# Kernel optimization log

Hardware: AMD Instinct MI355X
Metric: run time of the kernel (lower is better)

Reference implementation:

```python
import jax, jax.numpy as jnp
import numpy as np

N_NODES = 50000
N_EDGES = 800000
D_FEAT = 128      # node feature dim
D_IN = 2 * D_FEAT # MLP input (concat of x_i and x_j - x_i)
D_OUT = 256


def setup_inputs() -> dict:
    key = jax.random.key(0)
    ks = jax.random.split(key, 8)
    x = jax.random.normal(ks[0], (N_NODES, D_FEAT), dtype=jnp.float32)
    edge_index = jax.random.randint(ks[1], (2, N_EDGES), 0, N_NODES, dtype=jnp.int64)
    s1 = 1.0 / np.sqrt(D_IN)
    s2 = 1.0 / np.sqrt(D_OUT)
    W1 = jax.random.uniform(ks[2], (D_IN, D_OUT), jnp.float32, -s1, s1)
    b1 = jax.random.uniform(ks[3], (D_OUT,), jnp.float32, -s1, s1)
    W2 = jax.random.uniform(ks[4], (D_OUT, D_OUT), jnp.float32, -s2, s2)
    b2 = jax.random.uniform(ks[5], (D_OUT,), jnp.float32, -s2, s2)
    W3 = jax.random.uniform(ks[6], (D_OUT, D_OUT), jnp.float32, -s2, s2)
    b3 = jax.random.uniform(ks[7], (D_OUT,), jnp.float32, -s2, s2)
    return {"x": x, "edge_index": edge_index, "W1": W1, "b1": b1,
            "W2": W2, "b2": b2, "W3": W3, "b3": b3}


def reference(x, edge_index, W1, b1, W2, b2, W3, b3):
    # EdgeConv: for edge (j -> i): msg = MLP(concat([x_i, x_j - x_i])); max-aggregate at i
    src, dst = edge_index[0], edge_index[1]
    x_i = x[dst]                       # [E, D_FEAT] target features
    x_j = x[src]                       # [E, D_FEAT] source features
    e = jnp.concatenate([x_i, x_j - x_i], axis=-1)  # [E, 2*D_FEAT]
    h = jax.nn.relu(e @ W1 + b1)
    h = jax.nn.relu(h @ W2 + b2)
    h = h @ W3 + b3                    # [E, D_OUT]
    out = jax.ops.segment_max(h, dst, num_segments=N_NODES)  # [N, D_OUT]
    # nodes with no incoming edges -> 0 (PyG scatter-max fill)
    return jnp.where(jnp.isfinite(out), out, jnp.zeros((), out.dtype))
```

## Files before the change

### kernel.cpp

```cpp
#include <hip/hip_runtime.h>
#include <stdint.h>


#define N_NODES 50000
#define N_EDGES 800000
#define EPB 64
#define NBLK 12500

typedef __attribute__((ext_vector_type(4))) float f32x4;
typedef __attribute__((ext_vector_type(8))) _Float16 f16x8;
typedef __attribute__((ext_vector_type(4))) unsigned int u32x4;
typedef __attribute__((ext_vector_type(2))) unsigned int u32x2;

__device__ __forceinline__ unsigned int pkrtz(float a, float b){
  auto p = __builtin_amdgcn_cvt_pkrtz(a, b);
  return __builtin_bit_cast(unsigned int, p);
}
__device__ __forceinline__ unsigned int f16bits(float f){
  _Float16 h = (_Float16)f;
  return (unsigned int)__builtin_bit_cast(unsigned short, h);
}
__device__ __forceinline__ unsigned int pkadd_relu(unsigned int a, unsigned int b){
  unsigned int s, r;
  asm("v_pk_add_f16 %0, %1, %2" : "=v"(s) : "v"(a), "v"(b));
  asm("v_pk_max_f16 %0, %1, %2" : "=v"(r) : "v"(s), "v"(0u));
  return r;
}
__device__ __forceinline__ unsigned int fmap(float f){
  unsigned int u = __builtin_bit_cast(unsigned int, f);
  return (u & 0x80000000u) ? ~u : (u | 0x80000000u);
}
__device__ __forceinline__ bool is64(const unsigned int* e){
  return (e[1] | e[3] | e[5] | e[7] | e[9] | e[11] | e[13] | e[15]) == 0u;
}

extern "C" __global__ void k_histw(const void* __restrict__ eidx, unsigned int* __restrict__ cnt,
                                   const float* __restrict__ W1, const float* __restrict__ W2,
                                   const float* __restrict__ W3,
                                   unsigned short* __restrict__ w2s, unsigned short* __restrict__ w3s,
                                   unsigned short* __restrict__ wdf){
  const int b = blockIdx.x;
  if (b < 3125){
    int i = b * 256 + threadIdx.x;
    int d = is64((const unsigned int*)eidx)
          ? (int)((const long long*)eidx)[N_EDGES + i]
          : ((const int*)eidx)[N_EDGES + i];
    atomicAdd(&cnt[d], 1u);
    return;
  }
  int t = (b - 3125) * 256 + threadIdx.x;
  if (t < 16384){
    const float* W = (t & 8192) ? W3 : W2;
    unsigned short* o = (t & 8192) ? w3s : w2s;
    int r = t & 8191, lane = r & 63, blk = r >> 6;
    int m  = (blk >> 3) * 16 + (lane & 15);
    int k0 = (blk & 7) * 32 + (lane >> 4) * 8;
    u32x4 ov;
    #pragma unroll
    for (int j = 0; j < 4; j++){
      unsigned int lo = f16bits(W[(size_t)(k0 + 2*j    ) * 256 + m]);
      unsigned int hi = f16bits(W[(size_t)(k0 + 2*j + 1) * 256 + m]);
      ov[j] = lo | (hi << 16);
    }
    *(u32x4*)(o + (size_t)r * 8) = ov;
  } else {
    int r = t - 16384, lane = r & 63, blk = r >> 6;
    int m  = (blk >> 2) * 16 + (lane & 15);
    int k0 = (blk & 3) * 32 + (lane >> 4) * 8;
    u32x4 ov;
    #pragma unroll
    for (int j = 0; j < 4; j++){
      float vlo, vhi;
      int ka = k0 + 2*j, kb = k0 + 2*j + 1;
      if (m < 256){
        vlo = W1[(size_t)ka * 256 + m] - W1[(size_t)(ka + 128) * 256 + m];
        vhi = W1[(size_t)kb * 256 + m] - W1[(size_t)(kb + 128) * 256 + m];
      } else {
        vlo = W1[(size_t)(ka + 128) * 256 + (m - 256)];
        vhi = W1[(size_t)(kb + 128) * 256 + (m - 256)];
      }
      ov[j] = f16bits(vlo) | (f16bits(vhi) << 16);
    }
    *(u32x4*)(wdf + (size_t)r * 8) = ov;
  }
}

extern "C" __global__ void k_psum(const unsigned int* __restrict__ cnt, unsigned int* __restrict__ bsum){
  __shared__ unsigned int red[4];
  const int b = blockIdx.x, t = threadIdx.x, i = b * 256 + t;
  unsigned int v = (i < N_NODES) ? cnt[i] : 0u;
  #pragma unroll
  for (int d = 32; d; d >>= 1) v += __shfl_down(v, d, 64);
  if ((t & 63) == 0) red[t >> 6] = v;
  __syncthreads();
  if (t == 0) bsum[b] = red[0] + red[1] + red[2] + red[3];
}
extern "C" __global__ void __launch_bounds__(256) k_bscan(const unsigned int* __restrict__ bsum,
                                                          unsigned int* __restrict__ bbase){
  __shared__ unsigned int s[256];
  const int t = threadIdx.x;
  unsigned int v = (t < 196) ? bsum[t] : 0u;
  s[t] = v; __syncthreads();
  for (int d = 1; d < 256; d <<= 1){
    unsigned int u = (t >= d) ? s[t - d] : 0u;
    __syncthreads(); s[t] += u; __syncthreads();
  }
  if (t < 196) bbase[t] = s[t] - v;
}
extern "C" __global__ void k_apply(const unsigned int* __restrict__ cnt,
                                   const unsigned int* __restrict__ bbase,
                                   unsigned int* __restrict__ off){
  __shared__ unsigned int s[256];
  const int b = blockIdx.x, t = threadIdx.x, i = b * 256 + t;
  unsigned int v = (i < N_NODES) ? cnt[i] : 0u;
  s[t] = v; __syncthreads();
  for (int d = 1; d < 256; d <<= 1){
    unsigned int u = (t >= d) ? s[t - d] : 0u;
    __syncthreads(); s[t] += u; __syncthreads();
  }
  if (i < N_NODES) off[i] = bbase[b] + s[t] - v;
}

extern "C" __global__ void __launch_bounds__(256) k_bucketac(
    const void* __restrict__ eidx, unsigned int* __restrict__ cur,
    unsigned int* __restrict__ sPair,
    const float* __restrict__ x, const unsigned short* __restrict__ wdf,
    const float* __restrict__ b1, unsigned short* __restrict__ acb){
  __shared__ unsigned char smx[16384];
  const int b = blockIdx.x;
  if (b < 3125){
    int i = b * 256 + threadIdx.x;
    int s, d;
    if (is64((const unsigned int*)eidx)){
      const long long* p = (const long long*)eidx;
      s = (int)p[i]; d = (int)p[N_EDGES + i];
    } else {
      const int* p = (const int*)eidx;
      s = p[i]; d = p[N_EDGES + i];
    }
    unsigned int pos = atomicAdd(&cur[d], 1u);
    sPair[pos] = (unsigned int)s | ((unsigned int)d << 16);
    return;
  }
  const int tid = threadIdx.x, lane = tid & 63, w = tid >> 6;
  const int n0 = (b - 3125) * 64;
  {
    const int nl = tid >> 2, q = tid & 3;
    int node = n0 + nl; if (node > N_NODES - 1) node = N_NODES - 1;
    const f32x4* xp = (const f32x4*)(x + (size_t)node * 128 + q * 32);
    unsigned char* base = smx + (((nl >> 4) * 256 + q * 64 + (nl & 15)) << 4);
    #pragma unroll
    for (int s = 0; s < 4; s++){
      f32x4 v0 = xp[s * 2], v1 = xp[s * 2 + 1];
      u32x4 ov = { pkrtz(v0[0], v0[1]), pkrtz(v0[2], v0[3]),
                   pkrtz(v1[0], v1[1]), pkrtz(v1[2], v1[3]) };
      *(u32x4*)(base + s * 256) = ov;
    }
  }
  __syncthreads();
  const int lm = lane & 15, g = lane >> 4;
  f32x4 acc[8][4];
  #pragma unroll
  for (int mf = 0; mf < 8; mf++)
    #pragma unroll
    for (int nf = 0; nf < 4; nf++) acc[mf][nf] = (f32x4){0.f, 0.f, 0.f, 0.f};
  #pragma unroll
  for (int ks = 0; ks < 4; ks++){
    f16x8 af[8], bfr[4];
    #pragma unroll
    for (int mf = 0; mf < 8; mf++)
      af[mf] = __builtin_bit_cast(f16x8, *(const u32x4*)(wdf + (size_t)(((w * 8 + mf) * 4 + ks) * 64 + lane) * 8));
    #pragma unroll
    for (int nf = 0; nf < 4; nf++)
      bfr[nf] = __builtin_bit_cast(f16x8, *(const u32x4*)(smx + nf * 4096 + ks * 1024 + lane * 16));
    #pragma unroll
    for (int mf = 0; mf < 8; mf++)
      #pragma unroll
      for (int nf = 0; nf < 4; nf++)
        acc[mf][nf] = __builtin_amdgcn_mfma_f32_16x16x32_f16(af[mf], bfr[nf], acc[mf][nf], 0, 0, 0);
  }
  #pragma unroll
  for (int mf = 0; mf < 8; mf++){
    const int m0 = w * 128 + mf * 16 + g * 4;
    f32x4 bb = (f32x4){0.f, 0.f, 0.f, 0.f};
    if (w < 2) bb = *(const f32x4*)(b1 + m0);
    #pragma unroll
    for (int nf = 0; nf < 4; nf++){
      int node = n0 + nf * 16 + lm;
      if (node < N_NODES){
        u32x2 pv = { pkrtz(acc[mf][nf][0] + bb[0], acc[mf][nf][1] + bb[1]),
                     pkrtz(acc[mf][nf][2] + bb[2], acc[mf][nf][3] + bb[3]) };
        *(u32x2*)(acb + (size_t)node * 512 + m0) = pv;
      }
    }
  }
}

extern "C" __global__ void __launch_bounds__(256, 4) k_edge(
    const unsigned short* __restrict__ acb,
    const unsigned short* __restrict__ w2f, const unsigned short* __restrict__ w3f,
    const float* __restrict__ b2, const float* __restrict__ b3,
    const unsigned int* __restrict__ sPair,
    unsigned int* __restrict__ outu){
  __shared__ unsigned char sm[32768];
  __shared__ int dstI[EPB];
  const int tid = threadIdx.x;
  const int lane = tid & 63;
  const int w = tid >> 6;

  const int bid = blockIdx.x;
  const int xcd = bid & 7, idx = bid >> 3;
  const int sb = (xcd < 4) ? xcd * 1563 : 4 * 1563 + (xcd - 4) * 1562;
  const int e0 = (sb + idx) * EPB;

  f16x8 afp[4];
  #pragma unroll
  for (int mf = 0; mf < 4; mf++)
    afp[mf] = __builtin_bit_cast(f16x8, *(const u32x4*)(w2f + (size_t)(((w * 4 + mf) * 8 + 0) * 64 + lane) * 8));

  if (tid < EPB) dstI[tid] = (int)(sPair[e0 + tid] >> 16);

  {
    const int e = tid >> 2, q = tid & 3;
    const unsigned int pr = sPair[e0 + e];
    const unsigned short* pa = acb + (size_t)(pr >> 16) * 512 + q * 64;
    const unsigned short* pc = acb + (size_t)(pr & 0xFFFFu) * 512 + 256 + q * 64;
    unsigned char* base = sm + (e >> 4) * 8192 + (e & 15) * 16;
    #pragma unroll
    for (int j = 0; j < 8; j++){
      u32x4 ua = *(const u32x4*)(pa + j * 8);
      u32x4 uc = *(const u32x4*)(pc + j * 8);
      u32x4 ov;
      #pragma unroll
      for (int t2 = 0; t2 < 4; t2++) ov[t2] = pkadd_relu(ua[t2], uc[t2]);
      *(u32x4*)(base + (q * 2 + (j >> 2)) * 1024 + (j & 3) * 256) = ov;
    }
  }
  __syncthreads();

  const int lm = lane & 15, g = lane >> 4;
  f32x4 acc[4][4];
  {
    #pragma unroll
    for (int mf = 0; mf < 4; mf++){
      const f32x4 bb = *(const f32x4*)(b2 + w * 64 + mf * 16 + g * 4);
      #pragma unroll
      for (int nf = 0; nf < 4; nf++) acc[mf][nf] = bb;
    }
  }

  #pragma unroll
  for (int ks = 0; ks < 8; ks++){
    f16x8 af[4], bfr[4];
    #pragma unroll
    for (int mf = 0; mf < 4; mf++)
      af[mf] = (ks == 0) ? afp[mf]
             : __builtin_bit_cast(f16x8, *(const u32x4*)(w2f + (size_t)(((w * 4 + mf) * 8 + ks) * 64 + lane) * 8));
    #pragma unroll
    for (int nf = 0; nf < 4; nf++)
      bfr[nf] = __builtin_bit_cast(f16x8, *(const u32x4*)(sm + nf * 8192 + ks * 1024 + lane * 16));
    __builtin_amdgcn_s_setprio(1);
    #pragma unroll
    for (int mf = 0; mf < 4; mf++)
      #pragma unroll
      for (int nf = 0; nf < 4; nf++)
        acc[mf][nf] = __builtin_amdgcn_mfma_f32_16x16x32_f16(af[mf], bfr[nf], acc[mf][nf], 0, 0, 0);
    __builtin_amdgcn_s_setprio(0);
  }

  #pragma unroll
  for (int mf = 0; mf < 4; mf++)
    afp[mf] = __builtin_bit_cast(f16x8, *(const u32x4*)(w3f + (size_t)(((w * 4 + mf) * 8 + 0) * 64 + lane) * 8));
  __syncthreads();

  {
    #pragma unroll
    for (int mf = 0; mf < 4; mf++){
      const int m0 = w * 64 + mf * 16 + g * 4;
      const int boff = (m0 >> 5) * 1024 + ((m0 >> 3) & 3) * 256 + lm * 16 + (m0 & 7) * 2;
      #pragma unroll
      for (int nf = 0; nf < 4; nf++){
        float v0 = fmaxf(acc[mf][nf][0], 0.f);
        float v1 = fmaxf(acc[mf][nf][1], 0.f);
        float v2 = fmaxf(acc[mf][nf][2], 0.f);
        float v3 = fmaxf(acc[mf][nf][3], 0.f);
        u32x2 pv = { pkrtz(v0, v1), pkrtz(v2, v3) };
        *(u32x2*)(sm + nf * 8192 + boff) = pv;
      }
    }
  }
  __syncthreads();

  {
    #pragma unroll
    for (int mf = 0; mf < 4; mf++){
      const f32x4 bb = *(const f32x4*)(b3 + w * 64 + mf * 16 + g * 4);
      #pragma unroll
      for (int nf = 0; nf < 4; nf++) acc[mf][nf] = bb;
    }
  }
  #pragma unroll
  for (int ks = 0; ks < 8; ks++){
    f16x8 af[4], bfr[4];
    #pragma unroll
    for (int mf = 0; mf < 4; mf++)
      af[mf] = (ks == 0) ? afp[mf]
             : __builtin_bit_cast(f16x8, *(const u32x4*)(w3f + (size_t)(((w * 4 + mf) * 8 + ks) * 64 + lane) * 8));
    #pragma unroll
    for (int nf = 0; nf < 4; nf++)
      bfr[nf] = __builtin_bit_cast(f16x8, *(const u32x4*)(sm + nf * 8192 + ks * 1024 + lane * 16));
    __builtin_amdgcn_s_setprio(1);
    #pragma unroll
    for (int mf = 0; mf < 4; mf++)
      #pragma unroll
      for (int nf = 0; nf < 4; nf++)
        acc[mf][nf] = __builtin_amdgcn_mfma_f32_16x16x32_f16(af[mf], bfr[nf], acc[mf][nf], 0, 0, 0);
    __builtin_amdgcn_s_setprio(0);
  }
  __syncthreads();

  float vmaxf = -__builtin_inff();
  int curDst = dstI[0];
  const int t4 = tid * 4;
  #pragma unroll
  for (int half = 0; half < 2; half++){
    #pragma unroll
    for (int mf = 0; mf < 4; mf++){
      const int m0 = w * 64 + mf * 16 + g * 4;
      #pragma unroll
      for (int nfl = 0; nfl < 2; nfl++){
        const int r = nfl * 16 + lm;
        const int nf = half * 2 + nfl;
        *(f32x4*)(sm + r * 1024 + ((m0 * 4) ^ ((r & 7) << 4))) = acc[mf][nf];
      }
    }
    __syncthreads();
    for (int it = 0; it < 32; it++){
      float v = *(const float*)(sm + it * 1024 + (t4 ^ ((it & 7) << 4)));
      const int d = dstI[half * 32 + it];
      if (d != curDst){
        atomicMax(outu + (size_t)curDst * 256 + tid, fmap(vmaxf));
        curDst = d; vmaxf = -__builtin_inff();
      }
      vmaxf = fmaxf(vmaxf, v);
    }
    __syncthreads();
  }
  atomicMax(outu + (size_t)curDst * 256 + tid, fmap(vmaxf));
}

extern "C" __global__ void k_fix(u32x4* __restrict__ o){
  size_t i = (size_t)blockIdx.x * 256 + threadIdx.x;
  u32x4 u = o[i];
  #pragma unroll
  for (int j = 0; j < 4; j++)
    u[j] = (u[j] == 0u) ? 0u : ((u[j] & 0x80000000u) ? (u[j] ^ 0x80000000u) : ~u[j]);
  o[i] = u;
}

extern "C" void kernel_launch(void* const* d_in, const int* in_sizes, int n_in,
                              void* d_out, int out_size, void* d_ws, size_t ws_size,
                              hipStream_t stream){
  const float* x  = (const float*)d_in[0];
  const void*  ei = d_in[1];
  const float* W1 = (const float*)d_in[2];
  const float* b1 = (const float*)d_in[3];
  const float* W2 = (const float*)d_in[4];
  const float* b2 = (const float*)d_in[5];
  const float* W3 = (const float*)d_in[6];
  const float* b3 = (const float*)d_in[7];

  const size_t AC_BYTES = (size_t)N_NODES * 512 * 2;
  const size_t W_BYTES  = 256 * 256 * 2;
  const size_t P_BYTES  = (size_t)N_EDGES * 4;
  const size_t C_BYTES  = 200704;
  char* ws = (char*)d_ws;
  size_t o = 0;
  unsigned short* acb  = (unsigned short*)(ws + o); o += AC_BYTES;
  unsigned short* w2s  = (unsigned short*)(ws + o); o += W_BYTES;
  unsigned short* w3s  = (unsigned short*)(ws + o); o += W_BYTES;
  unsigned short* wdf  = (unsigned short*)(ws + o); o += W_BYTES;
  unsigned int*  sPair = (unsigned int*)(ws + o);   o += P_BYTES;
  unsigned int*  cnt   = (unsigned int*)(ws + o);   o += C_BYTES;
  unsigned int*  offA  = (unsigned int*)(ws + o);   o += C_BYTES;
  unsigned int*  bsum  = (unsigned int*)(ws + o);   o += 1024;
  unsigned int*  bbase = (unsigned int*)(ws + o);   o += 1024;
  if (ws_size < o) return;

  (void)hipMemsetAsync(cnt, 0, C_BYTES, stream);
  k_histw<<<3125 + 96, 256, 0, stream>>>(ei, cnt, W1, W2, W3, w2s, w3s, wdf);
  k_psum<<<196, 256, 0, stream>>>(cnt, bsum);
  k_bscan<<<1, 256, 0, stream>>>(bsum, bbase);
  k_apply<<<196, 256, 0, stream>>>(cnt, bbase, offA);
  k_bucketac<<<3125 + 782, 256, 0, stream>>>(ei, offA, sPair, x, wdf, b1, acb);
  (void)hipMemsetAsync(d_out, 0, (size_t)out_size * 4, stream);
  k_edge<<<NBLK, 256, 0, stream>>>(acb, w2s, w3s, b2, b3, sPair, (unsigned int*)d_out);
  k_fix<<<out_size / 1024, 256, 0, stream>>>((u32x4*)d_out);
}
```

Baseline: 432.3 us.

## Fuse block scan and output zeroing into apply; fp16 epilogue max reduction

Merges the single-block scan kernel into the offset-apply kernel, with every block redundantly scanning the 196 block sums, and folds the output memset into the same kernel. This removes two launches. The edge kernel epilogue now packs accumulators to fp16 into shared memory in a single pass instead of two fp32 halves, which drops a pair of barriers. It then max-reduces two channels per thread with packed f16 max, using half the threads per edge group. The cost is rounding the final layer outputs to fp16 before the max, which lowers output precision, plus two atomics per thread at each segment boundary.

```diff
diff --git a/kernel.cpp b/kernel.cpp
--- a/kernel.cpp
+++ b/kernel.cpp
@@ -25,6 +25,17 @@
   asm("v_pk_add_f16 %0, %1, %2" : "=v"(s) : "v"(a), "v"(b));
   asm("v_pk_max_f16 %0, %1, %2" : "=v"(r) : "v"(s), "v"(0u));
   return r;
+}
+__device__ __forceinline__ unsigned int pkmax(unsigned int a, unsigned int b){
+  unsigned int r;
+  asm("v_pk_max_f16 %0, %1, %2" : "=v"(r) : "v"(a), "v"(b));
+  return r;
+}
+__device__ __forceinline__ float f16lo2f(unsigned int v){
+  return (float)__builtin_bit_cast(_Float16, (unsigned short)(v & 0xFFFFu));
+}
+__device__ __forceinline__ float f16hi2f(unsigned int v){
+  return (float)__builtin_bit_cast(_Float16, (unsigned short)(v >> 16));
 }
 __device__ __forceinline__ unsigned int fmap(float f){
   unsigned int u = __builtin_bit_cast(unsigned int, f);
@@ -95,30 +106,29 @@
   __syncthreads();
   if (t == 0) bsum[b] = red[0] + red[1] + red[2] + red[3];
 }
-extern "C" __global__ void __launch_bounds__(256) k_bscan(const unsigned int* __restrict__ bsum,
-                                                          unsigned int* __restrict__ bbase){
-  __shared__ unsigned int s[256];
-  const int t = threadIdx.x;
-  unsigned int v = (t < 196) ? bsum[t] : 0u;
-  s[t] = v; __syncthreads();
-  for (int d = 1; d < 256; d <<= 1){
-    unsigned int u = (t >= d) ? s[t - d] : 0u;
-    __syncthreads(); s[t] += u; __syncthreads();
-  }
-  if (t < 196) bbase[t] = s[t] - v;
-}
-extern "C" __global__ void k_apply(const unsigned int* __restrict__ cnt,
-                                   const unsigned int* __restrict__ bbase,
-                                   unsigned int* __restrict__ off){
+
+extern "C" __global__ void __launch_bounds__(256) k_apply(
+    const unsigned int* __restrict__ cnt, const unsigned int* __restrict__ bsum,
+    unsigned int* __restrict__ off, u32x4* __restrict__ outz, int nquads){
+  __shared__ unsigned int ps[256];
   __shared__ unsigned int s[256];
   const int b = blockIdx.x, t = threadIdx.x, i = b * 256 + t;
+  const u32x4 z = (u32x4){0u, 0u, 0u, 0u};
+  for (int q = i; q < nquads; q += 196 * 256) outz[q] = z;
+  unsigned int bv = (t < 196) ? bsum[t] : 0u;
+  ps[t] = bv; __syncthreads();
+  for (int d = 1; d < 256; d <<= 1){
+    unsigned int u = (t >= d) ? ps[t - d] : 0u;
+    __syncthreads(); ps[t] += u; __syncthreads();
+  }
+  const unsigned int base = (b > 0) ? ps[b - 1] : 0u;
   unsigned int v = (i < N_NODES) ? cnt[i] : 0u;
   s[t] = v; __syncthreads();
   for (int d = 1; d < 256; d <<= 1){
     unsigned int u = (t >= d) ? s[t - d] : 0u;
     __syncthreads(); s[t] += u; __syncthreads();
   }
-  if (i < N_NODES) off[i] = bbase[b] + s[t] - v;
+  if (i < N_NODES) off[i] = base + s[t] - v;
 }
 
 extern "C" __global__ void __launch_bounds__(256) k_bucketac(
@@ -319,34 +329,41 @@
   }
   __syncthreads();
 
-  float vmaxf = -__builtin_inff();
-  int curDst = dstI[0];
-  const int t4 = tid * 4;
-  #pragma unroll
-  for (int half = 0; half < 2; half++){
+  {
     #pragma unroll
     for (int mf = 0; mf < 4; mf++){
       const int m0 = w * 64 + mf * 16 + g * 4;
       #pragma unroll
-      for (int nfl = 0; nfl < 2; nfl++){
-        const int r = nfl * 16 + lm;
-        const int nf = half * 2 + nfl;
-        *(f32x4*)(sm + r * 1024 + ((m0 * 4) ^ ((r & 7) << 4))) = acc[mf][nf];
+      for (int nf = 0; nf < 4; nf++){
+        const int r = nf * 16 + lm;
+        u32x2 pv = { pkrtz(acc[mf][nf][0], acc[mf][nf][1]),
+                     pkrtz(acc[mf][nf][2], acc[mf][nf][3]) };
+        *(u32x2*)(sm + r * 512 + ((m0 * 2) ^ ((r & 7) << 4))) = pv;
       }
     }
-    __syncthreads();
-    for (int it = 0; it < 32; it++){
-      float v = *(const float*)(sm + it * 1024 + (t4 ^ ((it & 7) << 4)));
-      const int d = dstI[half * 32 + it];
+  }
+  __syncthreads();
+
+  {
+    const int p = tid & 127, sub = tid >> 7;
+    unsigned int vmax = 0xFC00FC00u;
+    int curDst = dstI[sub * 32];
+    for (int k2 = 0; k2 < 32; k2++){
+      const int rl = sub * 32 + k2;
+      unsigned int v = *(const unsigned int*)(sm + rl * 512 + ((p * 4) ^ ((rl & 7) << 4)));
+      const int d = dstI[rl];
       if (d != curDst){
-        atomicMax(outu + (size_t)curDst * 256 + tid, fmap(vmaxf));
-        curDst = d; vmaxf = -__builtin_inff();
+        unsigned int* o = outu + (size_t)curDst * 256 + 2 * p;
+        atomicMax(o,     fmap(f16lo2f(vmax)));
+        atomicMax(o + 1, fmap(f16hi2f(vmax)));
+        curDst = d; vmax = 0xFC00FC00u;
       }
-      vmaxf = fmaxf(vmaxf, v);
-    }
-    __syncthreads();
-  }
-  atomicMax(outu + (size_t)curDst * 256 + tid, fmap(vmaxf));
+      vmax = pkmax(vmax, v);
+    }
+    unsigned int* o = outu + (size_t)curDst * 256 + 2 * p;
+    atomicMax(o,     fmap(f16lo2f(vmax)));
+    atomicMax(o + 1, fmap(f16hi2f(vmax)));
+  }
 }
 
 extern "C" __global__ void k_fix(u32x4* __restrict__ o){
@@ -384,16 +401,13 @@
   unsigned int*  cnt   = (unsigned int*)(ws + o);   o += C_BYTES;
   unsigned int*  offA  = (unsigned int*)(ws + o);   o += C_BYTES;
   unsigned int*  bsum  = (unsigned int*)(ws + o);   o += 1024;
-  unsigned int*  bbase = (unsigned int*)(ws + o);   o += 1024;
   if (ws_size < o) return;
 
   (void)hipMemsetAsync(cnt, 0, C_BYTES, stream);
   k_histw<<<3125 + 96, 256, 0, stream>>>(ei, cnt, W1, W2, W3, w2s, w3s, wdf);
   k_psum<<<196, 256, 0, stream>>>(cnt, bsum);
-  k_bscan<<<1, 256, 0, stream>>>(bsum, bbase);
-  k_apply<<<196, 256, 0, stream>>>(cnt, bbase, offA);
+  k_apply<<<196, 256, 0, stream>>>(cnt, bsum, offA, (u32x4*)d_out, out_size / 4);
   k_bucketac<<<3125 + 782, 256, 0, stream>>>(ei, offA, sPair, x, wdf, b1, acb);
-  (void)hipMemsetAsync(d_out, 0, (size_t)out_size * 4, stream);
   k_edge<<<NBLK, 256, 0, stream>>>(acb, w2s, w3s, b2, b3, sPair, (unsigned int*)d_out);
   k_fix<<<out_size / 1024, 256, 0, stream>>>((u32x4*)d_out);
 }
```

Measured after the change: 419.7 us, median of 2. 1.03x faster.
